# Performance work log

Hardware: AMD Instinct MI355X
Metric: run time of the kernel (lower is better)

## Reference

```python
import jax, jax.numpy as jnp
import numpy as np

N_E = 1024
E_DIM = 256
BETA = 0.25
B, L = 32, 1024


def setup_inputs() -> dict:
    key = jax.random.key(0)
    k1, k2 = jax.random.split(key)
    z = jax.random.normal(k1, (B, E_DIM, L), dtype=jnp.float32)
    mask = jnp.ones((B, L), dtype=jnp.float32)
    embedding = jax.random.uniform(k2, (N_E, E_DIM), dtype=jnp.float32,
                                   minval=-1.0 / N_E, maxval=1.0 / N_E)
    return {"z": z, "mask": mask, "embedding": embedding}


def reference(z, mask, embedding):
    # conv branch: (B, C, L) -> (B, L, C) -> (N, C)
    Bz, C, Lz = z.shape
    zp = jnp.transpose(z, (0, 2, 1))          # (B, L, C)
    zf = zp.reshape(-1, C)                    # (N, C)

    # squared L2 distance to every codebook entry: ||z||^2 + ||e||^2 - 2 z.e
    d = (jnp.sum(zf * zf, axis=1, keepdims=True)
         + jnp.sum(embedding * embedding, axis=1)
         - 2.0 * (zf @ embedding.T))          # (N, n_e)
    idx = jnp.argmin(d, axis=1)               # (N,)

    # gather == one_hot @ embedding
    z_q = embedding[idx].reshape(Bz, Lz, C)   # (B, L, C)

    m = mask[..., None]                       # (B, L, 1)
    commitment_loss = jnp.mean(((jax.lax.stop_gradient(z_q) - zp) * m) ** 2)
    codebook_loss = jnp.mean(((z_q - jax.lax.stop_gradient(zp)) * m) ** 2)
    loss = commitment_loss + BETA * codebook_loss

    # straight-through estimator
    z_q_st = zp + jax.lax.stop_gradient(z_q - zp)

    one_hot = jax.nn.one_hot(idx, N_E, dtype=zf.dtype)           # (N, n_e)
    e_mean = jnp.zeros((N_E,), zf.dtype).at[idx].add(1.0) / idx.shape[0]
    perplexity = jnp.exp(-jnp.sum(e_mean * jnp.log(e_mean + 1e-10)))

    z_q_out = jnp.transpose(z_q_st, (0, 2, 1))  # back to (B, C, L)
    return (loss, z_q_out, perplexity, one_hot, idx[:, None])
```

## Files before the change

### kernel.cpp

```cpp
#include <hip/hip_runtime.h>

constexpr int B_ = 32, C_ = 256, L_ = 1024, NE = 1024;
constexpr int NPTS = B_ * L_;
constexpr long long LOSS_OFF = 0;
constexpr long long ZQ_OFF   = 1;
constexpr long long PERP_OFF = 1 + 8388608;
constexpr long long OH_OFF   = PERP_OFF + 1;
constexpr long long IDX_OFF  = OH_OFF + 33554432LL;
constexpr size_t WS_IDX = 0;
constexpr size_t WS_CNT = 131072;
constexpr size_t WS_LP  = 135168;
constexpr size_t WS_E2  = 139264;

constexpr float MARGIN = 7e-4f;

typedef _Float16 f16x8 __attribute__((ext_vector_type(8)));
typedef float    f32x4 __attribute__((ext_vector_type(4)));

__device__ inline unsigned fkey(float f) {
  unsigned u = __float_as_uint(f);
  return (u & 0x80000000u) ? ~u : (u | 0x80000000u);
}
__device__ inline float unfkey(unsigned k) {
  unsigned u = (k & 0x80000000u) ? (k ^ 0x80000000u) : ~k;
  return __uint_as_float(u);
}

__global__ __launch_bounds__(64) void k_e2(const float* __restrict__ emb,
                                           float* __restrict__ e2) {
  const int j = blockIdx.x;
  const int t = threadIdx.x;
  const float* row = emb + (size_t)j * C_;
  double s = 0.0;
#pragma unroll
  for (int q = 0; q < 4; ++q) {
    float v = row[t + 64 * q];
    s += (double)v * (double)v;
  }
#pragma unroll
  for (int off = 32; off > 0; off >>= 1) s += __shfl_down(s, off);
  if (t == 0) e2[j] = (float)s;
}

__global__ __launch_bounds__(256) void k_ehl(const float* __restrict__ emb,
                                             _Float16* __restrict__ ehl) {
  const int i = blockIdx.x * 256 + threadIdx.x;
  float4 v = reinterpret_cast<const float4*>(emb)[i];
  _Float16 h0 = (_Float16)v.x, h1 = (_Float16)v.y;
  _Float16 h2 = (_Float16)v.z, h3 = (_Float16)v.w;
  unsigned u0 = (unsigned)__builtin_bit_cast(unsigned short, h0) |
                ((unsigned)__builtin_bit_cast(unsigned short, h1) << 16);
  unsigned u1 = (unsigned)__builtin_bit_cast(unsigned short, h2) |
                ((unsigned)__builtin_bit_cast(unsigned short, h3) << 16);
  reinterpret_cast<uint2*>(ehl)[i] = make_uint2(u0, u1);
}

__global__ __launch_bounds__(512, 2) void k_screen(const float* __restrict__ z,
                                                   const _Float16* __restrict__ ehl,
                                                   const float* __restrict__ e2g,
                                                   unsigned short* __restrict__ cand_codes,
                                                   unsigned* __restrict__ cand_cnt) {
  __shared__ _Float16 Az[128 * 256];
  __shared__ unsigned minkey[128];
  __shared__ unsigned ccnt[128];
  __shared__ unsigned short cand[128 * 32];

  const int tid  = threadIdx.x;
  const int lane = tid & 63;
  const int wid  = tid >> 6;
  const int wr   = wid >> 2;
  const int wc   = wid & 3;
  const int l15  = lane & 15;
  const int lhi  = lane >> 4;
  const int n0   = blockIdx.x * 128;
  const int b    = blockIdx.x >> 3;
  const int l0   = (blockIdx.x & 7) << 7;

  const uint4* ehl4 = reinterpret_cast<const uint4*>(ehl);

  {
    const float4* z4 = reinterpret_cast<const float4*>(z + (size_t)b * (C_ * L_) + l0);
    const int l4 = tid & 31;
    const int kp = tid >> 5;
#pragma unroll
    for (int rr = 0; rr < 8; ++rr) {
      const int k0 = rr * 32 + kp * 2;
      float4 a0 = z4[(size_t)k0 * (L_ / 4) + l4];
      float4 a1 = z4[(size_t)(k0 + 1) * (L_ / 4) + l4];
      const float av0[4] = {a0.x, a0.y, a0.z, a0.w};
      const float av1[4] = {a1.x, a1.y, a1.z, a1.w};
#pragma unroll
      for (int j = 0; j < 4; ++j) {
        _Float16 h0 = (_Float16)av0[j];
        _Float16 h1 = (_Float16)av1[j];
        unsigned pk = (unsigned)__builtin_bit_cast(unsigned short, h0) |
                      ((unsigned)__builtin_bit_cast(unsigned short, h1) << 16);
        const int p = l4 * 4 + j;
        const int slot = k0 >> 3;
        const int addr = p * 256 + ((slot ^ (p & 31)) << 3) + (k0 & 7);
        *reinterpret_cast<unsigned*>(&Az[addr]) = pk;
      }
    }
  }
  if (tid < 128) { minkey[tid] = 0xFFFFFFFFu; ccnt[tid] = 0u; }
  __syncthreads();

  f32x4 acc[4][4];
#pragma unroll
  for (int i = 0; i < 4; ++i)
#pragma unroll
    for (int j = 0; j < 4; ++j) acc[i][j] = (f32x4){0.f, 0.f, 0.f, 0.f};

  for (int ph = 0; ph < 8; ++ph) {
    const int cc = ph >> 1;
    const int kh = ph & 1;
#pragma unroll
    for (int s = 0; s < 4; ++s) {
      const int slotA = kh * 16 + s * 4 + lhi;
      f16x8 bfr[4];
#pragma unroll
      for (int tj = 0; tj < 4; ++tj)
        bfr[tj] = __builtin_bit_cast(f16x8,
            ehl4[(size_t)(cc * 256 + wc * 64 + tj * 16 + l15) * 32 +
                 kh * 16 + s * 4 + lhi]);
      f16x8 afr[4];
#pragma unroll
      for (int ti = 0; ti < 4; ++ti) {
        const int pA = wr * 64 + ti * 16 + l15;
        const int swzA = slotA ^ (((ti & 1) << 4) ^ l15);
        afr[ti] = *reinterpret_cast<const f16x8*>(&Az[pA * 256 + swzA * 8]);
      }
#pragma unroll
      for (int ti = 0; ti < 4; ++ti)
#pragma unroll
        for (int tj = 0; tj < 4; ++tj)
          acc[ti][tj] = __builtin_amdgcn_mfma_f32_16x16x32_f16(
              afr[ti], bfr[tj], acc[ti][tj], 0, 0, 0);
    }
    if (kh == 1) {
      float e2r[4];
#pragma unroll
      for (int tj = 0; tj < 4; ++tj)
        e2r[tj] = e2g[cc * 256 + wc * 64 + tj * 16 + l15];
#pragma unroll
      for (int ti = 0; ti < 4; ++ti) {
#pragma unroll
        for (int r = 0; r < 4; ++r) {
          float m = e2r[0] - 2.0f * acc[ti][0][r];
#pragma unroll
          for (int tj = 1; tj < 4; ++tj) {
            float v = e2r[tj] - 2.0f * acc[ti][tj][r];
            m = fminf(m, v);
          }
          m = fminf(m, __shfl_xor(m, 1));
          m = fminf(m, __shfl_xor(m, 2));
          m = fminf(m, __shfl_xor(m, 4));
          m = fminf(m, __shfl_xor(m, 8));
          if (l15 == 0) {
            const int p = wr * 64 + ti * 16 + lhi * 4 + r;
            atomicMin(&minkey[p], fkey(m));
          }
        }
      }
      __syncthreads();
#pragma unroll
      for (int ti = 0; ti < 4; ++ti) {
#pragma unroll
        for (int r = 0; r < 4; ++r) {
          const int p = wr * 64 + ti * 16 + lhi * 4 + r;
          const float thr = unfkey(minkey[p]) + MARGIN;
#pragma unroll
          for (int tj = 0; tj < 4; ++tj) {
            float s = e2r[tj] - 2.0f * acc[ti][tj][r];
            if (s <= thr) {
              unsigned pos = atomicAdd(&ccnt[p], 1u);
              if (pos < 32u)
                cand[p * 32 + pos] = (unsigned short)(cc * 256 + wc * 64 + tj * 16 + l15);
            }
          }
        }
      }
#pragma unroll
      for (int i = 0; i < 4; ++i)
#pragma unroll
        for (int j = 0; j < 4; ++j) acc[i][j] = (f32x4){0.f, 0.f, 0.f, 0.f};
    }
  }
  __syncthreads();

  if (tid < 128) {
    const int n = n0 + tid;
    cand_cnt[n] = ccnt[tid];
    const unsigned* src = reinterpret_cast<const unsigned*>(&cand[tid * 32]);
    unsigned* dst = reinterpret_cast<unsigned*>(cand_codes) + (size_t)n * 16;
#pragma unroll
    for (int q = 0; q < 16; ++q) dst[q] = src[q];
  }
}

__global__ __launch_bounds__(256, 2) void k_post(const float* __restrict__ z,
                                                 const float* __restrict__ emb,
                                                 const float* __restrict__ mask,
                                                 const float* __restrict__ e2g,
                                                 const unsigned short* __restrict__ cand_codes,
                                                 const unsigned* __restrict__ cand_cnt,
                                                 int* __restrict__ idxw,
                                                 unsigned* __restrict__ counts,
                                                 float* __restrict__ idx_out,
                                                 float* __restrict__ zq_out,
                                                 float* __restrict__ lp) {
  __shared__ float zs[256][34];
  __shared__ float eq[256][34];
  __shared__ unsigned long long bestkey[32];
  __shared__ float z2s[32];
  __shared__ int ids[32];
  __shared__ unsigned char dcnt[32];
  __shared__ int bad[32];
  __shared__ int nbad;
  __shared__ float red[256];
  __shared__ int rdi[256];

  const int tid = threadIdx.x, bid = blockIdx.x;
  const int b = bid >> 5, l0 = (bid & 31) << 5, n0 = bid << 5;

  {
    const float4* z4 = reinterpret_cast<const float4*>(z + (size_t)b * C_ * L_ + l0);
    const int l4 = tid & 7, kk = tid >> 3;
#pragma unroll
    for (int rep = 0; rep < 8; ++rep) {
      int k = rep * 32 + kk;
      float4 v = z4[(size_t)k * (L_ / 4) + l4];
      *reinterpret_cast<float4*>(&zs[k][l4 * 4]) = v;
    }
  }
  if (tid == 0) nbad = 0;
  __syncthreads();

  if (tid < 32) {
    const int n = n0 + tid;
    const unsigned cnt = cand_cnt[n];
    bestkey[tid] = ~0ULL;
    double s = 0.0;
#pragma unroll 8
    for (int k = 0; k < 256; ++k) {
      float v = zs[k][tid];
      s += (double)v * (double)v;
    }
    z2s[tid] = (float)s;
    if (cnt == 1u) {
      dcnt[tid] = 0;
      ids[tid] = cand_codes[(size_t)n * 32];
    } else if (cnt >= 2u && cnt <= 32u) {
      dcnt[tid] = (unsigned char)cnt;
    } else {
      dcnt[tid] = 0;
      bad[atomicAdd(&nbad, 1)] = tid;
    }
  }
  __syncthreads();

  {
    const int p = tid >> 3, j = tid & 7;
    const int cnt = dcnt[p];
    const int n = n0 + p;
    for (int q = j; q < cnt; q += 8) {
      const int c = cand_codes[(size_t)n * 32 + q];
      const float4* er = reinterpret_cast<const float4*>(emb + (size_t)c * C_);
      float acc = 0.f;
#pragma unroll 4
      for (int k4 = 0; k4 < 64; ++k4) {
        float4 e = er[k4];
        acc = fmaf(zs[k4 * 4 + 0][p], e.x, acc);
        acc = fmaf(zs[k4 * 4 + 1][p], e.y, acc);
        acc = fmaf(zs[k4 * 4 + 2][p], e.z, acc);
        acc = fmaf(zs[k4 * 4 + 3][p], e.w, acc);
      }
      const float d = (z2s[p] + e2g[c]) - 2.0f * acc;
      const unsigned long long key = ((unsigned long long)fkey(d) << 32) | (unsigned)c;
      atomicMin(&bestkey[p], key);
    }
  }
  __syncthreads();
  if (tid < 32 && dcnt[tid]) ids[tid] = (int)(unsigned)(bestkey[tid] & 0xFFFFFFFFu);

  if (nbad > 0) {
    __syncthreads();
    for (int ib = 0; ib < nbad; ++ib) {
      const int p = bad[ib];
      float bd = 3.4e38f;
      int bi = 0x7fffffff;
      for (int c = tid * 4; c < tid * 4 + 4; ++c) {
        const float* er = emb + (size_t)c * C_;
        float acc = 0.f;
        for (int k = 0; k < 256; ++k) acc = fmaf(zs[k][p], er[k], acc);
        const float d = (z2s[p] + e2g[c]) - 2.0f * acc;
        if (d < bd || (d == bd && c < bi)) { bd = d; bi = c; }
      }
      red[tid] = bd; rdi[tid] = bi;
      __syncthreads();
      for (int off = 128; off > 0; off >>= 1) {
        if (tid < off) {
          if (red[tid + off] < red[tid] ||
              (red[tid + off] == red[tid] && rdi[tid + off] < rdi[tid])) {
            red[tid] = red[tid + off]; rdi[tid] = rdi[tid + off];
          }
        }
        __syncthreads();
      }
      if (tid == 0) ids[p] = rdi[0];
      __syncthreads();
    }
  }
  __syncthreads();

  if (tid < 32) {
    const int n = n0 + tid;
    const int id = ids[tid];
    idxw[n] = id;
    idx_out[n] = (float)id;
    atomicAdd(&counts[id], 1u);
  }
  __syncthreads();

  {
    const int r = tid >> 3, kq = tid & 7;
    const float4* e4 = reinterpret_cast<const float4*>(emb + (size_t)ids[r] * C_);
#pragma unroll
    for (int rep = 0; rep < 8; ++rep) {
      int c4 = rep * 8 + kq;
      float4 v = e4[c4];
      eq[c4 * 4 + 0][r] = v.x;
      eq[c4 * 4 + 1][r] = v.y;
      eq[c4 * 4 + 2][r] = v.z;
      eq[c4 * 4 + 3][r] = v.w;
    }
  }
  __syncthreads();

  {
    const int lq = tid & 31, cg = tid >> 5;
    const float m = mask[b * L_ + l0 + lq];
    const size_t zbase = (size_t)b * C_ * L_ + l0 + lq;
    float s = 0.f;
#pragma unroll 4
    for (int ci = 0; ci < 32; ++ci) {
      int c = cg * 32 + ci;
      float zv = zs[c][lq];
      float q  = eq[c][lq];
      float diff = q - zv;
      zq_out[zbase + (size_t)c * L_] = zv + diff;
      float t = diff * m;
      s = fmaf(t, t, s);
    }
    red[tid] = s;
  }
  __syncthreads();
  for (int off = 128; off > 0; off >>= 1) {
    if (tid < off) red[tid] += red[tid + off];
    __syncthreads();
  }
  if (tid == 0) lp[bid] = red[0];
}

__global__ __launch_bounds__(256) void k_onehot(const int* __restrict__ idxw,
                                                float* __restrict__ oh) {
  const int tid = threadIdx.x, bid = blockIdx.x;
#pragma unroll
  for (int r = 0; r < 16; ++r) {
    const int n = bid * 16 + r;
    const int id = idxw[n];
    float* row = oh + (size_t)n * NE;
    const int c = tid * 4;
    float2 v0, v1;
    v0.x = (c + 0 == id) ? 1.f : 0.f;
    v0.y = (c + 1 == id) ? 1.f : 0.f;
    v1.x = (c + 2 == id) ? 1.f : 0.f;
    v1.y = (c + 3 == id) ? 1.f : 0.f;
    *reinterpret_cast<float2*>(row + c)     = v0;
    *reinterpret_cast<float2*>(row + c + 2) = v1;
  }
}

__global__ __launch_bounds__(256) void k_final(const float* __restrict__ lp,
                                               const unsigned int* __restrict__ counts,
                                               float* __restrict__ out) {
  __shared__ float red[256];
  const int t = threadIdx.x;
  red[t] = lp[t] + lp[t + 256] + lp[t + 512] + lp[t + 768];
  __syncthreads();
  for (int off = 128; off > 0; off >>= 1) {
    if (t < off) red[t] += red[t + off];
    __syncthreads();
  }
  if (t == 0) {
    float m = red[0] / 8388608.0f;
    out[LOSS_OFF] = m + 0.25f * m;
  }
  __syncthreads();
  float h = 0.f;
#pragma unroll
  for (int q = 0; q < 4; ++q) {
    int jj = t * 4 + q;
    float em = (float)counts[jj] * (1.0f / 32768.0f);
    h += em * logf(em + 1e-10f);
  }
  red[t] = h;
  __syncthreads();
  for (int off = 128; off > 0; off >>= 1) {
    if (t < off) red[t] += red[t + off];
    __syncthreads();
  }
  if (t == 0) out[PERP_OFF] = expf(-red[0]);
}

extern "C" void kernel_launch(void* const* d_in, const int* in_sizes, int n_in,
                              void* d_out, int out_size, void* d_ws, size_t ws_size,
                              hipStream_t stream) {
  const float* z    = (const float*)d_in[0];
  const float* mask = (const float*)d_in[1];
  const float* emb  = (const float*)d_in[2];
  float* out = (float*)d_out;
  char* ws = (char*)d_ws;
  int* idxw            = (int*)(ws + WS_IDX);
  unsigned int* counts = (unsigned int*)(ws + WS_CNT);
  float* lp            = (float*)(ws + WS_LP);
  float* e2            = (float*)(ws + WS_E2);

  uintptr_t sp = (uintptr_t)(out + OH_OFF);
  sp = (sp + 15) & ~(uintptr_t)15;
  _Float16* ehl              = (_Float16*)sp;
  unsigned short* cand_codes = (unsigned short*)(sp + 524288);
  unsigned* cand_cnt         = (unsigned*)(sp + 524288 + 2097152);

  hipMemsetAsync(counts, 0, NE * sizeof(unsigned int), stream);
  hipLaunchKernelGGL(k_e2, dim3(NE), dim3(64), 0, stream, emb, e2);
  hipLaunchKernelGGL(k_ehl, dim3(256), dim3(256), 0, stream, emb, ehl);
  hipLaunchKernelGGL(k_screen, dim3(256), dim3(512), 0, stream,
                     z, ehl, e2, cand_codes, cand_cnt);
  hipLaunchKernelGGL(k_post, dim3(1024), dim3(256), 0, stream,
                     z, emb, mask, e2, cand_codes, cand_cnt,
                     idxw, counts, out + IDX_OFF, out + ZQ_OFF, lp);
  hipLaunchKernelGGL(k_onehot, dim3(NPTS / 16), dim3(256), 0, stream,
                     idxw, out + OH_OFF);
  hipLaunchKernelGGL(k_final, dim3(1), dim3(256), 0, stream, lp, counts, out);
}
```

Measured before the change: 130.5 us.

## Fuse codebook prep kernels, halve screen tile to 64 points, parallelize z-norm

Merges the e2-norm, fp16 codebook conversion and counts memset into one prep kernel, cutting two launches and a memset. The screening kernel now covers 64 points per block instead of 128, doubling the grid to 512 blocks to fill the GPU's CUs, at the cost of reading the codebook B-fragments twice as often per point. In the post kernel, the per-point squared z norm is split across all 256 threads with a shared-memory partial reduction, where previously 32 threads did it serially.

```diff
diff --git a/kernel.cpp b/kernel.cpp
--- a/kernel.cpp
+++ b/kernel.cpp
@@ -26,33 +26,30 @@
   return __uint_as_float(u);
 }
 
-__global__ __launch_bounds__(64) void k_e2(const float* __restrict__ emb,
-                                           float* __restrict__ e2) {
-  const int j = blockIdx.x;
-  const int t = threadIdx.x;
-  const float* row = emb + (size_t)j * C_;
-  double s = 0.0;
-#pragma unroll
-  for (int q = 0; q < 4; ++q) {
-    float v = row[t + 64 * q];
-    s += (double)v * (double)v;
-  }
-#pragma unroll
-  for (int off = 32; off > 0; off >>= 1) s += __shfl_down(s, off);
-  if (t == 0) e2[j] = (float)s;
-}
-
-__global__ __launch_bounds__(256) void k_ehl(const float* __restrict__ emb,
-                                             _Float16* __restrict__ ehl) {
-  const int i = blockIdx.x * 256 + threadIdx.x;
-  float4 v = reinterpret_cast<const float4*>(emb)[i];
+__global__ __launch_bounds__(256) void k_prep(const float* __restrict__ emb,
+                                              _Float16* __restrict__ ehl,
+                                              float* __restrict__ e2,
+                                              unsigned* __restrict__ counts) {
+  const int tid = threadIdx.x, bid = blockIdx.x;
+  const int w = tid >> 6, lane = tid & 63;
+  const int code = bid * 4 + w;
+  float4 v = reinterpret_cast<const float4*>(emb + (size_t)code * C_)[lane];
   _Float16 h0 = (_Float16)v.x, h1 = (_Float16)v.y;
   _Float16 h2 = (_Float16)v.z, h3 = (_Float16)v.w;
   unsigned u0 = (unsigned)__builtin_bit_cast(unsigned short, h0) |
                 ((unsigned)__builtin_bit_cast(unsigned short, h1) << 16);
   unsigned u1 = (unsigned)__builtin_bit_cast(unsigned short, h2) |
                 ((unsigned)__builtin_bit_cast(unsigned short, h3) << 16);
-  reinterpret_cast<uint2*>(ehl)[i] = make_uint2(u0, u1);
+  reinterpret_cast<uint2*>(ehl)[code * 64 + lane] = make_uint2(u0, u1);
+  double s = 0.0;
+  s += (double)v.x * (double)v.x;
+  s += (double)v.y * (double)v.y;
+  s += (double)v.z * (double)v.z;
+  s += (double)v.w * (double)v.w;
+#pragma unroll
+  for (int off = 32; off > 0; off >>= 1) s += __shfl_down(s, off);
+  if (lane == 0) e2[code] = (float)s;
+  if (tid < 4) counts[bid * 4 + tid] = 0u;
 }
 
 __global__ __launch_bounds__(512, 2) void k_screen(const float* __restrict__ z,
@@ -60,10 +57,10 @@
                                                    const float* __restrict__ e2g,
                                                    unsigned short* __restrict__ cand_codes,
                                                    unsigned* __restrict__ cand_cnt) {
-  __shared__ _Float16 Az[128 * 256];
-  __shared__ unsigned minkey[128];
-  __shared__ unsigned ccnt[128];
-  __shared__ unsigned short cand[128 * 32];
+  __shared__ _Float16 Az[64 * 256];
+  __shared__ unsigned minkey[64];
+  __shared__ unsigned ccnt[64];
+  __shared__ unsigned short cand[64 * 32];
 
   const int tid  = threadIdx.x;
   const int lane = tid & 63;
@@ -72,19 +69,19 @@
   const int wc   = wid & 3;
   const int l15  = lane & 15;
   const int lhi  = lane >> 4;
-  const int n0   = blockIdx.x * 128;
-  const int b    = blockIdx.x >> 3;
-  const int l0   = (blockIdx.x & 7) << 7;
+  const int n0   = blockIdx.x * 64;
+  const int b    = blockIdx.x >> 4;
+  const int l0   = (blockIdx.x & 15) << 6;
 
   const uint4* ehl4 = reinterpret_cast<const uint4*>(ehl);
 
   {
     const float4* z4 = reinterpret_cast<const float4*>(z + (size_t)b * (C_ * L_) + l0);
-    const int l4 = tid & 31;
-    const int kp = tid >> 5;
-#pragma unroll
-    for (int rr = 0; rr < 8; ++rr) {
-      const int k0 = rr * 32 + kp * 2;
+    const int l4 = tid & 15;
+    const int kp = tid >> 4;
+#pragma unroll
+    for (int rr = 0; rr < 4; ++rr) {
+      const int k0 = rr * 64 + kp * 2;
       float4 a0 = z4[(size_t)k0 * (L_ / 4) + l4];
       float4 a1 = z4[(size_t)(k0 + 1) * (L_ / 4) + l4];
       const float av0[4] = {a0.x, a0.y, a0.z, a0.w};
@@ -102,12 +99,12 @@
       }
     }
   }
-  if (tid < 128) { minkey[tid] = 0xFFFFFFFFu; ccnt[tid] = 0u; }
-  __syncthreads();
-
-  f32x4 acc[4][4];
-#pragma unroll
-  for (int i = 0; i < 4; ++i)
+  if (tid < 64) { minkey[tid] = 0xFFFFFFFFu; ccnt[tid] = 0u; }
+  __syncthreads();
+
+  f32x4 acc[2][4];
+#pragma unroll
+  for (int i = 0; i < 2; ++i)
 #pragma unroll
     for (int j = 0; j < 4; ++j) acc[i][j] = (f32x4){0.f, 0.f, 0.f, 0.f};
 
@@ -123,15 +120,15 @@
         bfr[tj] = __builtin_bit_cast(f16x8,
             ehl4[(size_t)(cc * 256 + wc * 64 + tj * 16 + l15) * 32 +
                  kh * 16 + s * 4 + lhi]);
-      f16x8 afr[4];
-#pragma unroll
-      for (int ti = 0; ti < 4; ++ti) {
-        const int pA = wr * 64 + ti * 16 + l15;
-        const int swzA = slotA ^ (((ti & 1) << 4) ^ l15);
+      f16x8 afr[2];
+#pragma unroll
+      for (int ti = 0; ti < 2; ++ti) {
+        const int pA = wr * 32 + ti * 16 + l15;
+        const int swzA = slotA ^ ((ti << 4) ^ l15);
         afr[ti] = *reinterpret_cast<const f16x8*>(&Az[pA * 256 + swzA * 8]);
       }
 #pragma unroll
-      for (int ti = 0; ti < 4; ++ti)
+      for (int ti = 0; ti < 2; ++ti)
 #pragma unroll
         for (int tj = 0; tj < 4; ++tj)
           acc[ti][tj] = __builtin_amdgcn_mfma_f32_16x16x32_f16(
@@ -143,7 +140,7 @@
       for (int tj = 0; tj < 4; ++tj)
         e2r[tj] = e2g[cc * 256 + wc * 64 + tj * 16 + l15];
 #pragma unroll
-      for (int ti = 0; ti < 4; ++ti) {
+      for (int ti = 0; ti < 2; ++ti) {
 #pragma unroll
         for (int r = 0; r < 4; ++r) {
           float m = e2r[0] - 2.0f * acc[ti][0][r];
@@ -157,17 +154,17 @@
           m = fminf(m, __shfl_xor(m, 4));
           m = fminf(m, __shfl_xor(m, 8));
           if (l15 == 0) {
-            const int p = wr * 64 + ti * 16 + lhi * 4 + r;
+            const int p = wr * 32 + ti * 16 + lhi * 4 + r;
             atomicMin(&minkey[p], fkey(m));
           }
         }
       }
       __syncthreads();
 #pragma unroll
-      for (int ti = 0; ti < 4; ++ti) {
+      for (int ti = 0; ti < 2; ++ti) {
 #pragma unroll
         for (int r = 0; r < 4; ++r) {
-          const int p = wr * 64 + ti * 16 + lhi * 4 + r;
+          const int p = wr * 32 + ti * 16 + lhi * 4 + r;
           const float thr = unfkey(minkey[p]) + MARGIN;
 #pragma unroll
           for (int tj = 0; tj < 4; ++tj) {
@@ -181,14 +178,14 @@
         }
       }
 #pragma unroll
-      for (int i = 0; i < 4; ++i)
+      for (int i = 0; i < 2; ++i)
 #pragma unroll
         for (int j = 0; j < 4; ++j) acc[i][j] = (f32x4){0.f, 0.f, 0.f, 0.f};
     }
   }
   __syncthreads();
 
-  if (tid < 128) {
+  if (tid < 64) {
     const int n = n0 + tid;
     cand_cnt[n] = ccnt[tid];
     const unsigned* src = reinterpret_cast<const unsigned*>(&cand[tid * 32]);
@@ -211,6 +208,7 @@
                                                  float* __restrict__ lp) {
   __shared__ float zs[256][34];
   __shared__ float eq[256][34];
+  __shared__ double zpart[32][9];
   __shared__ unsigned long long bestkey[32];
   __shared__ float z2s[32];
   __shared__ int ids[32];
@@ -236,17 +234,26 @@
   if (tid == 0) nbad = 0;
   __syncthreads();
 
+  {
+    const int p = tid >> 3, j = tid & 7;
+    double s = 0.0;
+#pragma unroll 8
+    for (int k = j * 32; k < j * 32 + 32; ++k) {
+      float v = zs[k][p];
+      s += (double)v * (double)v;
+    }
+    zpart[p][j] = s;
+  }
+  __syncthreads();
+
   if (tid < 32) {
     const int n = n0 + tid;
+    double s = 0.0;
+#pragma unroll
+    for (int j = 0; j < 8; ++j) s += zpart[tid][j];
+    z2s[tid] = (float)s;
+    bestkey[tid] = ~0ULL;
     const unsigned cnt = cand_cnt[n];
-    bestkey[tid] = ~0ULL;
-    double s = 0.0;
-#pragma unroll 8
-    for (int k = 0; k < 256; ++k) {
-      float v = zs[k][tid];
-      s += (double)v * (double)v;
-    }
-    z2s[tid] = (float)s;
     if (cnt == 1u) {
       dcnt[tid] = 0;
       ids[tid] = cand_codes[(size_t)n * 32];
@@ -432,10 +439,9 @@
   unsigned short* cand_codes = (unsigned short*)(sp + 524288);
   unsigned* cand_cnt         = (unsigned*)(sp + 524288 + 2097152);
 
-  hipMemsetAsync(counts, 0, NE * sizeof(unsigned int), stream);
-  hipLaunchKernelGGL(k_e2, dim3(NE), dim3(64), 0, stream, emb, e2);
-  hipLaunchKernelGGL(k_ehl, dim3(256), dim3(256), 0, stream, emb, ehl);
-  hipLaunchKernelGGL(k_screen, dim3(256), dim3(512), 0, stream,
+  hipLaunchKernelGGL(k_prep, dim3(256), dim3(256), 0, stream,
+                     emb, ehl, e2, counts);
+  hipLaunchKernelGGL(k_screen, dim3(512), dim3(512), 0, stream,
                      z, ehl, e2, cand_codes, cand_cnt);
   hipLaunchKernelGGL(k_post, dim3(1024), dim3(256), 0, stream,
                      z, emb, mask, e2, cand_codes, cand_cnt,
```

Measured after the change: 135.7 us. +4.0%, slower.

## Fuse candidate rescoring into screen kernel and split zq/loss into separate pass

Applied to the files above, without the earlier changes.

Moves the exact fp32 rescoring of the screened candidates into the MFMA screening kernel. This removes the global round trip of candidate codes and counts, and the z-norm computation moves into the tile load. The fp16 codebook is re-laid out so each MFMA B-fragment load reads a contiguous 16-code group, and the counts memset is folded into the e2 prep kernel. A new k_zq_loss kernel handles 64 points per block, and the block-partial count that k_final sums is halved to 512. In exchange, the screen kernel now needs much more shared memory (occupancy bound drops to 1 block per SM), rescoring reads z from global with strided accesses, and the fallback path serialises over every bad point.

```diff
diff --git a/kernel.cpp b/kernel.cpp
--- a/kernel.cpp
+++ b/kernel.cpp
@@ -26,8 +26,30 @@
   return __uint_as_float(u);
 }
 
-__global__ __launch_bounds__(64) void k_e2(const float* __restrict__ emb,
-                                           float* __restrict__ e2) {
+__global__ __launch_bounds__(256) void k_prep_ehl(const float* __restrict__ emb,
+                                                  uint4* __restrict__ ehlF) {
+  const int u = blockIdx.x * 256 + threadIdx.x;
+  const int c16 = u & 15;
+  const int s8  = (u >> 4) & 31;
+  const int g   = u >> 9;
+  const int code = g * 16 + c16;
+  const float4* e4 = reinterpret_cast<const float4*>(emb + (size_t)code * C_) + s8 * 2;
+  float4 v0 = e4[0], v1 = e4[1];
+  const float f[8] = {v0.x, v0.y, v0.z, v0.w, v1.x, v1.y, v1.z, v1.w};
+  unsigned w[4];
+#pragma unroll
+  for (int i = 0; i < 4; ++i) {
+    _Float16 h0 = (_Float16)f[2 * i];
+    _Float16 h1 = (_Float16)f[2 * i + 1];
+    w[i] = (unsigned)__builtin_bit_cast(unsigned short, h0) |
+           ((unsigned)__builtin_bit_cast(unsigned short, h1) << 16);
+  }
+  ehlF[u] = make_uint4(w[0], w[1], w[2], w[3]);
+}
+
+__global__ __launch_bounds__(64) void k_prep_e2(const float* __restrict__ emb,
+                                                float* __restrict__ e2,
+                                                unsigned* __restrict__ counts) {
   const int j = blockIdx.x;
   const int t = threadIdx.x;
   const float* row = emb + (size_t)j * C_;
@@ -39,31 +61,27 @@
   }
 #pragma unroll
   for (int off = 32; off > 0; off >>= 1) s += __shfl_down(s, off);
-  if (t == 0) e2[j] = (float)s;
-}
-
-__global__ __launch_bounds__(256) void k_ehl(const float* __restrict__ emb,
-                                             _Float16* __restrict__ ehl) {
-  const int i = blockIdx.x * 256 + threadIdx.x;
-  float4 v = reinterpret_cast<const float4*>(emb)[i];
-  _Float16 h0 = (_Float16)v.x, h1 = (_Float16)v.y;
-  _Float16 h2 = (_Float16)v.z, h3 = (_Float16)v.w;
-  unsigned u0 = (unsigned)__builtin_bit_cast(unsigned short, h0) |
-                ((unsigned)__builtin_bit_cast(unsigned short, h1) << 16);
-  unsigned u1 = (unsigned)__builtin_bit_cast(unsigned short, h2) |
-                ((unsigned)__builtin_bit_cast(unsigned short, h3) << 16);
-  reinterpret_cast<uint2*>(ehl)[i] = make_uint2(u0, u1);
-}
-
-__global__ __launch_bounds__(512, 2) void k_screen(const float* __restrict__ z,
-                                                   const _Float16* __restrict__ ehl,
-                                                   const float* __restrict__ e2g,
-                                                   unsigned short* __restrict__ cand_codes,
-                                                   unsigned* __restrict__ cand_cnt) {
+  if (t == 0) { e2[j] = (float)s; counts[j] = 0u; }
+}
+
+__global__ __launch_bounds__(512, 1) void k_screen_rr(const float* __restrict__ z,
+                                                      const float* __restrict__ emb,
+                                                      const uint4* __restrict__ ehlF,
+                                                      const float* __restrict__ e2g,
+                                                      int* __restrict__ idxw,
+                                                      unsigned* __restrict__ counts,
+                                                      float* __restrict__ idx_out) {
   __shared__ _Float16 Az[128 * 256];
+  __shared__ double zpart[128][17];
+  __shared__ unsigned short cand[128 * 32];
+  __shared__ unsigned long long bestkey[128];
   __shared__ unsigned minkey[128];
   __shared__ unsigned ccnt[128];
-  __shared__ unsigned short cand[128 * 32];
+  __shared__ float z2s[128];
+  __shared__ int ids[128];
+  __shared__ unsigned char dcnt[128];
+  __shared__ float zcol[256];
+  __shared__ int nbad;
 
   const int tid  = threadIdx.x;
   const int lane = tid & 63;
@@ -76,12 +94,11 @@
   const int b    = blockIdx.x >> 3;
   const int l0   = (blockIdx.x & 7) << 7;
 
-  const uint4* ehl4 = reinterpret_cast<const uint4*>(ehl);
-
   {
     const float4* z4 = reinterpret_cast<const float4*>(z + (size_t)b * (C_ * L_) + l0);
     const int l4 = tid & 31;
     const int kp = tid >> 5;
+    double sj[4] = {0.0, 0.0, 0.0, 0.0};
 #pragma unroll
     for (int rr = 0; rr < 8; ++rr) {
       const int k0 = rr * 32 + kp * 2;
@@ -99,10 +116,15 @@
         const int slot = k0 >> 3;
         const int addr = p * 256 + ((slot ^ (p & 31)) << 3) + (k0 & 7);
         *reinterpret_cast<unsigned*>(&Az[addr]) = pk;
-      }
-    }
+        sj[j] += (double)av0[j] * (double)av0[j];
+        sj[j] += (double)av1[j] * (double)av1[j];
+      }
+    }
+#pragma unroll
+    for (int j = 0; j < 4; ++j) zpart[l4 * 4 + j][kp] = sj[j];
   }
   if (tid < 128) { minkey[tid] = 0xFFFFFFFFu; ccnt[tid] = 0u; }
+  if (tid == 0) nbad = 0;
   __syncthreads();
 
   f32x4 acc[4][4];
@@ -117,12 +139,13 @@
 #pragma unroll
     for (int s = 0; s < 4; ++s) {
       const int slotA = kh * 16 + s * 4 + lhi;
+      const int slotB = kh * 16 + s * 4 + lhi;
       f16x8 bfr[4];
 #pragma unroll
-      for (int tj = 0; tj < 4; ++tj)
-        bfr[tj] = __builtin_bit_cast(f16x8,
-            ehl4[(size_t)(cc * 256 + wc * 64 + tj * 16 + l15) * 32 +
-                 kh * 16 + s * 4 + lhi]);
+      for (int tj = 0; tj < 4; ++tj) {
+        const int g = cc * 16 + wc * 4 + tj;
+        bfr[tj] = __builtin_bit_cast(f16x8, ehlF[(g * 32 + slotB) * 16 + l15]);
+      }
       f16x8 afr[4];
 #pragma unroll
       for (int ti = 0; ti < 4; ++ti) {
@@ -189,145 +212,97 @@
   __syncthreads();
 
   if (tid < 128) {
-    const int n = n0 + tid;
-    cand_cnt[n] = ccnt[tid];
-    const unsigned* src = reinterpret_cast<const unsigned*>(&cand[tid * 32]);
-    unsigned* dst = reinterpret_cast<unsigned*>(cand_codes) + (size_t)n * 16;
-#pragma unroll
-    for (int q = 0; q < 16; ++q) dst[q] = src[q];
-  }
-}
-
-__global__ __launch_bounds__(256, 2) void k_post(const float* __restrict__ z,
-                                                 const float* __restrict__ emb,
-                                                 const float* __restrict__ mask,
-                                                 const float* __restrict__ e2g,
-                                                 const unsigned short* __restrict__ cand_codes,
-                                                 const unsigned* __restrict__ cand_cnt,
-                                                 int* __restrict__ idxw,
-                                                 unsigned* __restrict__ counts,
-                                                 float* __restrict__ idx_out,
-                                                 float* __restrict__ zq_out,
-                                                 float* __restrict__ lp) {
-  __shared__ float zs[256][34];
-  __shared__ float eq[256][34];
-  __shared__ unsigned long long bestkey[32];
-  __shared__ float z2s[32];
-  __shared__ int ids[32];
-  __shared__ unsigned char dcnt[32];
-  __shared__ int bad[32];
-  __shared__ int nbad;
-  __shared__ float red[256];
-  __shared__ int rdi[256];
-
-  const int tid = threadIdx.x, bid = blockIdx.x;
-  const int b = bid >> 5, l0 = (bid & 31) << 5, n0 = bid << 5;
-
-  {
-    const float4* z4 = reinterpret_cast<const float4*>(z + (size_t)b * C_ * L_ + l0);
-    const int l4 = tid & 7, kk = tid >> 3;
-#pragma unroll
-    for (int rep = 0; rep < 8; ++rep) {
-      int k = rep * 32 + kk;
-      float4 v = z4[(size_t)k * (L_ / 4) + l4];
-      *reinterpret_cast<float4*>(&zs[k][l4 * 4]) = v;
-    }
-  }
-  if (tid == 0) nbad = 0;
-  __syncthreads();
-
-  if (tid < 32) {
-    const int n = n0 + tid;
-    const unsigned cnt = cand_cnt[n];
+    double s = 0.0;
+#pragma unroll
+    for (int kp = 0; kp < 16; ++kp) s += zpart[tid][kp];
+    z2s[tid] = (float)s;
     bestkey[tid] = ~0ULL;
-    double s = 0.0;
-#pragma unroll 8
-    for (int k = 0; k < 256; ++k) {
-      float v = zs[k][tid];
-      s += (double)v * (double)v;
-    }
-    z2s[tid] = (float)s;
+    const unsigned cnt = ccnt[tid];
     if (cnt == 1u) {
       dcnt[tid] = 0;
-      ids[tid] = cand_codes[(size_t)n * 32];
-    } else if (cnt >= 2u && cnt <= 32u) {
+      ids[tid] = cand[tid * 32];
+    } else if (cnt <= 32u) {
       dcnt[tid] = (unsigned char)cnt;
     } else {
-      dcnt[tid] = 0;
-      bad[atomicAdd(&nbad, 1)] = tid;
+      dcnt[tid] = 0xFF;
+      atomicAdd(&nbad, 1);
     }
   }
   __syncthreads();
 
   {
-    const int p = tid >> 3, j = tid & 7;
-    const int cnt = dcnt[p];
-    const int n = n0 + p;
-    for (int q = j; q < cnt; q += 8) {
-      const int c = cand_codes[(size_t)n * 32 + q];
+    const int p = tid >> 2, j = tid & 3;
+    const int cnt = (dcnt[p] == 0xFF) ? 0 : (int)dcnt[p];
+    const float* zc = z + (size_t)b * (C_ * L_) + l0 + p;
+    for (int q = j; q < cnt; q += 4) {
+      const int c = cand[p * 32 + q];
       const float4* er = reinterpret_cast<const float4*>(emb + (size_t)c * C_);
-      float acc = 0.f;
+      float acc2 = 0.f;
 #pragma unroll 4
       for (int k4 = 0; k4 < 64; ++k4) {
         float4 e = er[k4];
-        acc = fmaf(zs[k4 * 4 + 0][p], e.x, acc);
-        acc = fmaf(zs[k4 * 4 + 1][p], e.y, acc);
-        acc = fmaf(zs[k4 * 4 + 2][p], e.z, acc);
-        acc = fmaf(zs[k4 * 4 + 3][p], e.w, acc);
-      }
-      const float d = (z2s[p] + e2g[c]) - 2.0f * acc;
-      const unsigned long long key = ((unsigned long long)fkey(d) << 32) | (unsigned)c;
+        acc2 = fmaf(zc[(size_t)(k4 * 4 + 0) * L_], e.x, acc2);
+        acc2 = fmaf(zc[(size_t)(k4 * 4 + 1) * L_], e.y, acc2);
+        acc2 = fmaf(zc[(size_t)(k4 * 4 + 2) * L_], e.z, acc2);
+        acc2 = fmaf(zc[(size_t)(k4 * 4 + 3) * L_], e.w, acc2);
+      }
+      const float d = (z2s[p] + e2g[c]) - 2.0f * acc2;
+      const unsigned long long key =
+          ((unsigned long long)fkey(d) << 32) | (unsigned)c;
       atomicMin(&bestkey[p], key);
     }
   }
   __syncthreads();
-  if (tid < 32 && dcnt[tid]) ids[tid] = (int)(unsigned)(bestkey[tid] & 0xFFFFFFFFu);
 
   if (nbad > 0) {
-    __syncthreads();
-    for (int ib = 0; ib < nbad; ++ib) {
-      const int p = bad[ib];
-      float bd = 3.4e38f;
-      int bi = 0x7fffffff;
-      for (int c = tid * 4; c < tid * 4 + 4; ++c) {
+    for (int p = 0; p < 128; ++p) {
+      if (dcnt[p] != 0xFF) continue;
+      const float* zc = z + (size_t)b * (C_ * L_) + l0 + p;
+      if (tid < 256) zcol[tid] = zc[(size_t)tid * L_];
+      __syncthreads();
+#pragma unroll
+      for (int h = 0; h < 2; ++h) {
+        const int c = tid * 2 + h;
         const float* er = emb + (size_t)c * C_;
-        float acc = 0.f;
-        for (int k = 0; k < 256; ++k) acc = fmaf(zs[k][p], er[k], acc);
-        const float d = (z2s[p] + e2g[c]) - 2.0f * acc;
-        if (d < bd || (d == bd && c < bi)) { bd = d; bi = c; }
-      }
-      red[tid] = bd; rdi[tid] = bi;
+        float acc2 = 0.f;
+        for (int k = 0; k < 256; ++k) acc2 = fmaf(zcol[k], er[k], acc2);
+        const float d = (z2s[p] + e2g[c]) - 2.0f * acc2;
+        const unsigned long long key =
+            ((unsigned long long)fkey(d) << 32) | (unsigned)c;
+        atomicMin(&bestkey[p], key);
+      }
       __syncthreads();
-      for (int off = 128; off > 0; off >>= 1) {
-        if (tid < off) {
-          if (red[tid + off] < red[tid] ||
-              (red[tid + off] == red[tid] && rdi[tid + off] < rdi[tid])) {
-            red[tid] = red[tid + off]; rdi[tid] = rdi[tid + off];
-          }
-        }
-        __syncthreads();
-      }
-      if (tid == 0) ids[p] = rdi[0];
-      __syncthreads();
-    }
-  }
-  __syncthreads();
-
-  if (tid < 32) {
+    }
+  }
+
+  if (tid < 128) {
     const int n = n0 + tid;
-    const int id = ids[tid];
+    int id = ids[tid];
+    if (dcnt[tid] != 0) id = (int)(unsigned)(bestkey[tid] & 0xFFFFFFFFu);
     idxw[n] = id;
     idx_out[n] = (float)id;
     atomicAdd(&counts[id], 1u);
   }
-  __syncthreads();
-
+}
+
+__global__ __launch_bounds__(256) void k_zq_loss(const float* __restrict__ z,
+                                                 const float* __restrict__ emb,
+                                                 const float* __restrict__ mask,
+                                                 const int* __restrict__ idxw,
+                                                 float* __restrict__ zq_out,
+                                                 float* __restrict__ lp) {
+  __shared__ float eq[256][66];
+  __shared__ float red[256];
+  const int tid = threadIdx.x, bid = blockIdx.x;
+  const int b = bid >> 4, l0 = (bid & 15) << 6, n0 = bid << 6;
   {
-    const int r = tid >> 3, kq = tid & 7;
-    const float4* e4 = reinterpret_cast<const float4*>(emb + (size_t)ids[r] * C_);
-#pragma unroll
-    for (int rep = 0; rep < 8; ++rep) {
-      int c4 = rep * 8 + kq;
+    const int r  = tid >> 2;
+    const int kq = tid & 3;
+    const int id = idxw[n0 + r];
+    const float4* e4 = reinterpret_cast<const float4*>(emb + (size_t)id * C_);
+#pragma unroll
+    for (int rep = 0; rep < 16; ++rep) {
+      int c4 = rep * 4 + kq;
       float4 v = e4[c4];
       eq[c4 * 4 + 0][r] = v.x;
       eq[c4 * 4 + 1][r] = v.y;
@@ -336,24 +311,21 @@
     }
   }
   __syncthreads();
-
-  {
-    const int lq = tid & 31, cg = tid >> 5;
-    const float m = mask[b * L_ + l0 + lq];
-    const size_t zbase = (size_t)b * C_ * L_ + l0 + lq;
-    float s = 0.f;
+  const int lq = tid & 63, cg = tid >> 6;
+  const float m = mask[b * L_ + l0 + lq];
+  const size_t zbase = (size_t)b * C_ * L_ + l0 + lq;
+  float s = 0.f;
 #pragma unroll 4
-    for (int ci = 0; ci < 32; ++ci) {
-      int c = cg * 32 + ci;
-      float zv = zs[c][lq];
-      float q  = eq[c][lq];
-      float diff = q - zv;
-      zq_out[zbase + (size_t)c * L_] = zv + diff;
-      float t = diff * m;
-      s = fmaf(t, t, s);
-    }
-    red[tid] = s;
-  }
+  for (int ci = 0; ci < 64; ++ci) {
+    int c = cg * 64 + ci;
+    float zv = z[zbase + (size_t)c * L_];
+    float q  = eq[c][lq];
+    float diff = q - zv;
+    zq_out[zbase + (size_t)c * L_] = zv + diff;
+    float t = diff * m;
+    s = fmaf(t, t, s);
+  }
+  red[tid] = s;
   __syncthreads();
   for (int off = 128; off > 0; off >>= 1) {
     if (tid < off) red[tid] += red[tid + off];
@@ -386,7 +358,7 @@
                                                float* __restrict__ out) {
   __shared__ float red[256];
   const int t = threadIdx.x;
-  red[t] = lp[t] + lp[t + 256] + lp[t + 512] + lp[t + 768];
+  red[t] = lp[t] + lp[t + 256];
   __syncthreads();
   for (int off = 128; off > 0; off >>= 1) {
     if (t < off) red[t] += red[t + off];
@@ -428,18 +400,14 @@
 
   uintptr_t sp = (uintptr_t)(out + OH_OFF);
   sp = (sp + 15) & ~(uintptr_t)15;
-  _Float16* ehl              = (_Float16*)sp;
-  unsigned short* cand_codes = (unsigned short*)(sp + 524288);
-  unsigned* cand_cnt         = (unsigned*)(sp + 524288 + 2097152);
-
-  hipMemsetAsync(counts, 0, NE * sizeof(unsigned int), stream);
-  hipLaunchKernelGGL(k_e2, dim3(NE), dim3(64), 0, stream, emb, e2);
-  hipLaunchKernelGGL(k_ehl, dim3(256), dim3(256), 0, stream, emb, ehl);
-  hipLaunchKernelGGL(k_screen, dim3(256), dim3(512), 0, stream,
-                     z, ehl, e2, cand_codes, cand_cnt);
-  hipLaunchKernelGGL(k_post, dim3(1024), dim3(256), 0, stream,
-                     z, emb, mask, e2, cand_codes, cand_cnt,
-                     idxw, counts, out + IDX_OFF, out + ZQ_OFF, lp);
+  uint4* ehlF = (uint4*)sp;
+
+  hipLaunchKernelGGL(k_prep_ehl, dim3(128), dim3(256), 0, stream, emb, ehlF);
+  hipLaunchKernelGGL(k_prep_e2, dim3(NE), dim3(64), 0, stream, emb, e2, counts);
+  hipLaunchKernelGGL(k_screen_rr, dim3(256), dim3(512), 0, stream,
+                     z, emb, ehlF, e2, idxw, counts, out + IDX_OFF);
+  hipLaunchKernelGGL(k_zq_loss, dim3(512), dim3(256), 0, stream,
+                     z, emb, mask, idxw, out + ZQ_OFF, lp);
   hipLaunchKernelGGL(k_onehot, dim3(NPTS / 16), dim3(256), 0, stream,
                      idxw, out + OH_OFF);
   hipLaunchKernelGGL(k_final, dim3(1), dim3(256), 0, stream, lp, counts, out);
```

After: 117.6 us. -9.9%, faster.
